# Optimization experiments

Hardware: AMD Instinct MI355X
Metric: run time of the kernel (lower is better)

## Reference

```python
import jax, jax.numpy as jnp
import numpy as np

N_NODES = 50000
N_EDGES = 800000
IN_DIM = 128
HID = 64
OUT = 64
HEADS = 4
NEG_SLOPE = 0.2  # DGL GATConv default leaky_relu negative slope


def gat_conv(x, src, dst, W, attn_l, attn_r, bias, n_heads, d_out, n_nodes):
    """DGL-style GATConv: x [N, F_in] -> [N, H, D]."""
    feat = (x @ W).reshape(n_nodes, n_heads, d_out)            # [N,H,D]
    el = jnp.sum(feat * attn_l, axis=-1)                        # [N,H]
    er = jnp.sum(feat * attn_r, axis=-1)                        # [N,H]
    e = jax.nn.leaky_relu(el[src] + er[dst], NEG_SLOPE)         # [E,H]
    # edge softmax over incoming edges of each dst node
    emax = jax.ops.segment_max(e, dst, num_segments=n_nodes)    # [N,H]
    emax = jnp.where(jnp.isfinite(emax), emax, 0.0)
    emax = jax.lax.stop_gradient(emax)
    a = jnp.exp(e - emax[dst])                                  # [E,H]
    denom = jax.ops.segment_sum(a, dst, num_segments=n_nodes)   # [N,H]
    alpha = a / jnp.maximum(denom[dst], 1e-9)                   # [E,H]
    msg = feat[src] * alpha[:, :, None]                         # [E,H,D]
    out = jax.ops.segment_sum(msg, dst, num_segments=n_nodes)   # [N,H,D]
    return out + bias.reshape(1, n_heads, d_out)


def setup_inputs() -> dict:
    key = jax.random.key(0)
    ks = jax.random.split(key, 12)
    features = jax.random.normal(ks[0], (N_NODES, IN_DIM), jnp.float32)
    src = jax.random.randint(ks[1], (N_EDGES,), 0, N_NODES)
    dst = jax.random.randint(ks[2], (N_EDGES,), 0, N_NODES)
    s1 = 1.0 / np.sqrt(IN_DIM)
    s2 = 1.0 / np.sqrt(HID * HEADS)
    return {
        "features": features,
        "src": src,
        "dst": dst,
        "W1": jax.random.normal(ks[3], (IN_DIM, HEADS * HID), jnp.float32) * s1,
        "al1": jax.random.normal(ks[4], (HEADS, HID), jnp.float32) * s1,
        "ar1": jax.random.normal(ks[5], (HEADS, HID), jnp.float32) * s1,
        "b1": jnp.zeros((HEADS * HID,), jnp.float32),
        "W2": jax.random.normal(ks[6], (HEADS * HID, HEADS * OUT), jnp.float32) * s2,
        "al2": jax.random.normal(ks[7], (HEADS, OUT), jnp.float32) * s2,
        "ar2": jax.random.normal(ks[8], (HEADS, OUT), jnp.float32) * s2,
        "b2": jnp.zeros((HEADS * OUT,), jnp.float32),
    }


def reference(features, src, dst, W1, al1, ar1, b1, W2, al2, ar2, b2):
    h = gat_conv(features, src, dst, W1, al1, ar1, b1, HEADS, HID, N_NODES)
    h = jax.nn.elu(h)                        # layer1 activation=F.elu
    h = h.reshape(N_NODES, HEADS * HID)      # .flatten(1)
    # dropout(0.2) is identity in eval mode
    h = gat_conv(h, src, dst, W2, al2, ar2, b2, HEADS, OUT, N_NODES)
    return h.mean(axis=1)                    # mean over heads -> [N, OUT]
```

## Files before the change

kernel.cpp:

```cpp
#include <hip/hip_runtime.h>
#include <hip/hip_bf16.h>
#include <math.h>

#define N_NODES 50000
#define N_EDGES 800000
#define IN_DIM 128
#define NEG_SLOPE 0.2f

typedef __attribute__((ext_vector_type(8))) short s16x8;
typedef __attribute__((ext_vector_type(4))) float f32x4;

__device__ inline unsigned short f2bf(float v) {
    unsigned u = __float_as_uint(v);
    unsigned r = (u + 0x7fffu + ((u >> 16) & 1u)) >> 16;
    return (unsigned short)r;
}
__device__ inline float bf2f(unsigned short b) {
    return __uint_as_float(((unsigned)b) << 16);
}
__device__ inline float lrelu(float v) {
    return v >= 0.f ? v : NEG_SLOPE * v;
}


__global__ void zero_int(int* __restrict__ p, int n) {
    int i = blockIdx.x * blockDim.x + threadIdx.x;
    if (i < n) p[i] = 0;
}

__global__ void hist_kernel(const int* __restrict__ dst, int* __restrict__ cnt) {
    int e = blockIdx.x * blockDim.x + threadIdx.x;
    if (e < N_EDGES) atomicAdd(&cnt[dst[e]], 1);
}

__global__ __launch_bounds__(1024) void scan_kernel(const int* __restrict__ cnt,
                                                    int* __restrict__ off, int n) {
    __shared__ int wsum[16];
    __shared__ int carry_s;
    int tid = threadIdx.x, wid = tid >> 6, lane = tid & 63;
    if (tid == 0) carry_s = 0;
    __syncthreads();
    for (int base = 0; base < n; base += 1024) {
        int i = base + tid;
        int v = (i < n) ? cnt[i] : 0;
        int x = v;
#pragma unroll
        for (int s = 1; s < 64; s <<= 1) {
            int t = __shfl_up(x, s, 64);
            if (lane >= s) x += t;
        }
        if (lane == 63) wsum[wid] = x;
        __syncthreads();
        if (wid == 0 && lane < 16) {
            int w = wsum[lane];
#pragma unroll
            for (int s = 1; s < 16; s <<= 1) {
                int t = __shfl_up(w, s, 64);
                if (lane >= s) w += t;
            }
            wsum[lane] = w;
        }
        __syncthreads();
        int woff = (wid > 0) ? wsum[wid - 1] : 0;
        int incl = carry_s + woff + x;
        if (i < n) off[i] = incl - v;
        __syncthreads();
        if (tid == 1023) carry_s = incl;
        __syncthreads();
    }
    if (threadIdx.x == 0) off[n] = carry_s;
}

__global__ void copy_int(const int* __restrict__ a, int* __restrict__ b, int n) {
    int i = blockIdx.x * blockDim.x + threadIdx.x;
    if (i < n) b[i] = a[i];
}

__global__ void scatter_kernel(const int* __restrict__ src, const int* __restrict__ dst,
                               int* __restrict__ cur, int* __restrict__ csr_src) {
    int e = blockIdx.x * blockDim.x + threadIdx.x;
    if (e < N_EDGES) {
        int d = dst[e];
        int pos = atomicAdd(&cur[d], 1);
        csr_src[pos] = src[e];
    }
}

template <int K>
__global__ void split_wt(const float* __restrict__ W, unsigned short* __restrict__ Bth,
                         unsigned short* __restrict__ Btl) {
    int k = blockIdx.x;
    int c = threadIdx.x;
    float v = W[(size_t)k * 256 + c];
    unsigned short h = f2bf(v);
    Bth[(size_t)c * K + k] = h;
    Btl[(size_t)c * K + k] = f2bf(v - bf2f(h));
}


template <int K, bool AF32>
__global__ __launch_bounds__(256) void mfma_gemm(const void* __restrict__ A_,
                                                 const unsigned short* __restrict__ Alo,
                                                 const unsigned short* __restrict__ Bth,
                                                 const unsigned short* __restrict__ Btl,
                                                 const float* __restrict__ attl,
                                                 const float* __restrict__ attr,
                                                 unsigned short* __restrict__ Chi,
                                                 float* __restrict__ el,
                                                 float* __restrict__ er,
                                                 int M) {
    int h = threadIdx.x >> 6;
    int lane = threadIdx.x & 63;
    int r = lane & 15;
    int g = lane >> 4;
    int kg = g * 8;
    int row0 = blockIdx.x * 32;

    f32x4 acc[2][4] = {};

    int rowA0 = row0 + r;      if (rowA0 >= M) rowA0 = M - 1;
    int rowA1 = row0 + 16 + r; if (rowA1 >= M) rowA1 = M - 1;

    const float* Af = (const float*)A_;
    const unsigned short* Ah = (const unsigned short*)A_;
    const unsigned short* pbh = Bth + (size_t)(h * 64 + r) * K + kg;
    const unsigned short* pbl = Btl + (size_t)(h * 64 + r) * K + kg;

#pragma unroll
    for (int kb = 0; kb < K; kb += 32) {
        s16x8 ah0, ah1, al0, al1;
        if (AF32) {
            const float* p0 = Af + (size_t)rowA0 * K + kb + kg;
            const float* p1 = Af + (size_t)rowA1 * K + kb + kg;
            float4 f00 = *reinterpret_cast<const float4*>(p0);
            float4 f01 = *reinterpret_cast<const float4*>(p0 + 4);
            float4 f10 = *reinterpret_cast<const float4*>(p1);
            float4 f11 = *reinterpret_cast<const float4*>(p1 + 4);
            float v0[8] = {f00.x, f00.y, f00.z, f00.w, f01.x, f01.y, f01.z, f01.w};
            float v1[8] = {f10.x, f10.y, f10.z, f10.w, f11.x, f11.y, f11.z, f11.w};
#pragma unroll
            for (int i = 0; i < 8; i++) {
                unsigned short hh0 = f2bf(v0[i]);
                unsigned short hh1 = f2bf(v1[i]);
                ah0[i] = (short)hh0; al0[i] = (short)f2bf(v0[i] - bf2f(hh0));
                ah1[i] = (short)hh1; al1[i] = (short)f2bf(v1[i] - bf2f(hh1));
            }
        } else {
            ah0 = *reinterpret_cast<const s16x8*>(Ah  + (size_t)rowA0 * K + kb + kg);
            ah1 = *reinterpret_cast<const s16x8*>(Ah  + (size_t)rowA1 * K + kb + kg);
            al0 = *reinterpret_cast<const s16x8*>(Alo + (size_t)rowA0 * K + kb + kg);
            al1 = *reinterpret_cast<const s16x8*>(Alo + (size_t)rowA1 * K + kb + kg);
        }
        s16x8 bh[4], bl[4];
#pragma unroll
        for (int ni = 0; ni < 4; ni++) {
            bh[ni] = *reinterpret_cast<const s16x8*>(pbh + (size_t)(ni * 16) * K + kb);
            bl[ni] = *reinterpret_cast<const s16x8*>(pbl + (size_t)(ni * 16) * K + kb);
        }
#pragma unroll
        for (int ni = 0; ni < 4; ni++) {
            acc[0][ni] = __builtin_amdgcn_mfma_f32_16x16x32_bf16(ah0, bh[ni], acc[0][ni], 0, 0, 0);
            acc[1][ni] = __builtin_amdgcn_mfma_f32_16x16x32_bf16(ah1, bh[ni], acc[1][ni], 0, 0, 0);
            acc[0][ni] = __builtin_amdgcn_mfma_f32_16x16x32_bf16(ah0, bl[ni], acc[0][ni], 0, 0, 0);
            acc[1][ni] = __builtin_amdgcn_mfma_f32_16x16x32_bf16(ah1, bl[ni], acc[1][ni], 0, 0, 0);
            acc[0][ni] = __builtin_amdgcn_mfma_f32_16x16x32_bf16(al0, bh[ni], acc[0][ni], 0, 0, 0);
            acc[1][ni] = __builtin_amdgcn_mfma_f32_16x16x32_bf16(al1, bh[ni], acc[1][ni], 0, 0, 0);
        }
    }

    float alv[4], arv[4];
#pragma unroll
    for (int ni = 0; ni < 4; ni++) {
        alv[ni] = attl[h * 64 + ni * 16 + r];
        arv[ni] = attr[h * 64 + ni * 16 + r];
    }
#pragma unroll
    for (int mi = 0; mi < 2; mi++) {
#pragma unroll
        for (int reg = 0; reg < 4; reg++) {
            int row = row0 + mi * 16 + g * 4 + reg;
            bool ok = row < M;
            float pel = 0.f, per_ = 0.f;
#pragma unroll
            for (int ni = 0; ni < 4; ni++) {
                float v = acc[mi][ni][reg];
                pel += v * alv[ni];
                per_ += v * arv[ni];
                if (ok) Chi[(size_t)row * 256 + h * 64 + ni * 16 + r] = f2bf(v);
            }
#pragma unroll
            for (int s = 1; s < 16; s <<= 1) {
                pel  += __shfl_xor(pel, s, 64);
                per_ += __shfl_xor(per_, s, 64);
            }
            if (r == 0 && ok) {
                el[row * 4 + h] = pel;
                er[row * 4 + h] = per_;
            }
        }
    }
}


template <int LAYER>
__global__ __launch_bounds__(256) void agg_kernel(const unsigned short* __restrict__ feat16,
                                                  const float* __restrict__ el,
                                                  const float* __restrict__ er,
                                                  const int* __restrict__ row_off,
                                                  const int* __restrict__ csr_src,
                                                  const float* __restrict__ bias,
                                                  unsigned short* __restrict__ out_hi,
                                                  unsigned short* __restrict__ out_lo,
                                                  float* __restrict__ outf) {
    int n = blockIdx.x * 4 + (threadIdx.x >> 6);
    int lane = threadIdx.x & 63;
    int h = lane >> 4;
    int js = row_off[n], je = row_off[n + 1];
    float er_nh = er[n * 4 + h];
    float m = -INFINITY, ssum = 0.f;
    float4 acc = make_float4(0.f, 0.f, 0.f, 0.f);
    int j = js;
    for (; j + 3 < je; j += 4) {
        int s0 = csr_src[j], s1 = csr_src[j + 1], s2 = csr_src[j + 2], s3 = csr_src[j + 3];
        ushort4 u0 = *reinterpret_cast<const ushort4*>(&feat16[(size_t)s0 * 256 + lane * 4]);
        ushort4 u1 = *reinterpret_cast<const ushort4*>(&feat16[(size_t)s1 * 256 + lane * 4]);
        ushort4 u2 = *reinterpret_cast<const ushort4*>(&feat16[(size_t)s2 * 256 + lane * 4]);
        ushort4 u3 = *reinterpret_cast<const ushort4*>(&feat16[(size_t)s3 * 256 + lane * 4]);
        float v0 = lrelu(el[s0 * 4 + h] + er_nh);
        float v1 = lrelu(el[s1 * 4 + h] + er_nh);
        float v2 = lrelu(el[s2 * 4 + h] + er_nh);
        float v3 = lrelu(el[s3 * 4 + h] + er_nh);
        float mx = fmaxf(fmaxf(v0, v1), fmaxf(v2, v3));
        float mn = fmaxf(m, mx);
        float sc = __expf(m - mn);
        float p0 = __expf(v0 - mn);
        float p1 = __expf(v1 - mn);
        float p2 = __expf(v2 - mn);
        float p3 = __expf(v3 - mn);
        ssum = ssum * sc + ((p0 + p1) + (p2 + p3));
        acc.x = acc.x * sc + (p0 * bf2f(u0.x) + p1 * bf2f(u1.x)) + (p2 * bf2f(u2.x) + p3 * bf2f(u3.x));
        acc.y = acc.y * sc + (p0 * bf2f(u0.y) + p1 * bf2f(u1.y)) + (p2 * bf2f(u2.y) + p3 * bf2f(u3.y));
        acc.z = acc.z * sc + (p0 * bf2f(u0.z) + p1 * bf2f(u1.z)) + (p2 * bf2f(u2.z) + p3 * bf2f(u3.z));
        acc.w = acc.w * sc + (p0 * bf2f(u0.w) + p1 * bf2f(u1.w)) + (p2 * bf2f(u2.w) + p3 * bf2f(u3.w));
        m = mn;
    }
    for (; j < je; j++) {
        int s = csr_src[j];
        ushort4 u = *reinterpret_cast<const ushort4*>(&feat16[(size_t)s * 256 + lane * 4]);
        float val = lrelu(el[s * 4 + h] + er_nh);
        float mn = fmaxf(m, val);
        float sc = __expf(m - mn);
        float p = __expf(val - mn);
        ssum = ssum * sc + p;
        acc.x = acc.x * sc + p * bf2f(u.x);
        acc.y = acc.y * sc + p * bf2f(u.y);
        acc.z = acc.z * sc + p * bf2f(u.z);
        acc.w = acc.w * sc + p * bf2f(u.w);
        m = mn;
    }
    float inv = 1.f / fmaxf(ssum, 1e-9f);
    float4 res;
    res.x = acc.x * inv + bias[lane * 4 + 0];
    res.y = acc.y * inv + bias[lane * 4 + 1];
    res.z = acc.z * inv + bias[lane * 4 + 2];
    res.w = acc.w * inv + bias[lane * 4 + 3];
    if (LAYER == 1) {
        res.x = res.x > 0.f ? res.x : __expf(res.x) - 1.f;
        res.y = res.y > 0.f ? res.y : __expf(res.y) - 1.f;
        res.z = res.z > 0.f ? res.z : __expf(res.z) - 1.f;
        res.w = res.w > 0.f ? res.w : __expf(res.w) - 1.f;
        ushort4 hz, lz;
        hz.x = f2bf(res.x); lz.x = f2bf(res.x - bf2f(hz.x));
        hz.y = f2bf(res.y); lz.y = f2bf(res.y - bf2f(hz.y));
        hz.z = f2bf(res.z); lz.z = f2bf(res.z - bf2f(hz.z));
        hz.w = f2bf(res.w); lz.w = f2bf(res.w - bf2f(hz.w));
        *reinterpret_cast<ushort4*>(&out_hi[(size_t)n * 256 + lane * 4]) = hz;
        *reinterpret_cast<ushort4*>(&out_lo[(size_t)n * 256 + lane * 4]) = lz;
    } else {
#pragma unroll
        for (int mask = 16; mask <= 32; mask <<= 1) {
            res.x += __shfl_xor(res.x, mask, 64);
            res.y += __shfl_xor(res.y, mask, 64);
            res.z += __shfl_xor(res.z, mask, 64);
            res.w += __shfl_xor(res.w, mask, 64);
        }
        if (lane < 16) {
            float4 o = make_float4(res.x * 0.25f, res.y * 0.25f, res.z * 0.25f, res.w * 0.25f);
            *reinterpret_cast<float4*>(&outf[(size_t)n * 64 + lane * 4]) = o;
        }
    }
}


extern "C" void kernel_launch(void* const* d_in, const int* in_sizes, int n_in,
                              void* d_out, int out_size, void* d_ws, size_t ws_size,
                              hipStream_t stream) {
    const float* features = (const float*)d_in[0];
    const int*   src      = (const int*)d_in[1];
    const int*   dst      = (const int*)d_in[2];
    const float* W1       = (const float*)d_in[3];
    const float* al1      = (const float*)d_in[4];
    const float* ar1      = (const float*)d_in[5];
    const float* b1       = (const float*)d_in[6];
    const float* W2       = (const float*)d_in[7];
    const float* al2      = (const float*)d_in[8];
    const float* ar2      = (const float*)d_in[9];
    const float* b2       = (const float*)d_in[10];
    float* out = (float*)d_out;

    char* ws = (char*)d_ws;
    unsigned short* feat16  = (unsigned short*)(ws);
    unsigned short* h1_hi   = (unsigned short*)(ws + 25600000);
    unsigned short* h1_lo   = (unsigned short*)(ws + 51200000);
    unsigned short* Bt1_hi  = (unsigned short*)(ws + 76800000);
    unsigned short* Bt1_lo  = (unsigned short*)(ws + 76865536);
    unsigned short* Bt2_hi  = (unsigned short*)(ws + 76931072);
    unsigned short* Bt2_lo  = (unsigned short*)(ws + 77062144);
    float*          el      = (float*)(ws + 77193216);
    float*          er      = (float*)(ws + 77993216);
    int*            row_off = (int*)  (ws + 78793216);
    int*            cur     = (int*)  (ws + 78993280);
    int*            csr     = (int*)  (ws + 79193280);

    zero_int<<<(N_NODES + 255) / 256, 256, 0, stream>>>(cur, N_NODES);
    hist_kernel<<<(N_EDGES + 255) / 256, 256, 0, stream>>>(dst, cur);
    scan_kernel<<<1, 1024, 0, stream>>>(cur, row_off, N_NODES);
    copy_int<<<(N_NODES + 255) / 256, 256, 0, stream>>>(row_off, cur, N_NODES);
    scatter_kernel<<<(N_EDGES + 255) / 256, 256, 0, stream>>>(src, dst, cur, csr);

    split_wt<IN_DIM><<<IN_DIM, 256, 0, stream>>>(W1, Bt1_hi, Bt1_lo);
    split_wt<256><<<256, 256, 0, stream>>>(W2, Bt2_hi, Bt2_lo);

    int gemm_blocks = (N_NODES + 31) / 32;

    mfma_gemm<IN_DIM, true><<<gemm_blocks, 256, 0, stream>>>(
        features, nullptr, Bt1_hi, Bt1_lo, al1, ar1, feat16, el, er, N_NODES);
    agg_kernel<1><<<12500, 256, 0, stream>>>(feat16, el, er, row_off, csr, b1, h1_hi, h1_lo, nullptr);

    mfma_gemm<256, false><<<gemm_blocks, 256, 0, stream>>>(
        h1_hi, h1_lo, Bt2_hi, Bt2_lo, al2, ar2, feat16, el, er, N_NODES);
    agg_kernel<2><<<12500, 256, 0, stream>>>(feat16, el, er, row_off, csr, b2, nullptr, nullptr, out);
}
```

Measured before the change: 398.5 us.

## Stage GEMM tiles in double-buffered LDS, pre-split features, unroll aggregation by eight

```diff
diff --git a/kernel.cpp b/kernel.cpp
--- a/kernel.cpp
+++ b/kernel.cpp
@@ -86,6 +86,22 @@
     }
 }
 
+
+__global__ void split_feat(const float* __restrict__ in, unsigned short* __restrict__ hi,
+                           unsigned short* __restrict__ lo, int n4) {
+    int i = blockIdx.x * blockDim.x + threadIdx.x;
+    if (i < n4) {
+        float4 v = *reinterpret_cast<const float4*>(&in[i * 4]);
+        ushort4 h, l;
+        h.x = f2bf(v.x); l.x = f2bf(v.x - bf2f(h.x));
+        h.y = f2bf(v.y); l.y = f2bf(v.y - bf2f(h.y));
+        h.z = f2bf(v.z); l.z = f2bf(v.z - bf2f(h.z));
+        h.w = f2bf(v.w); l.w = f2bf(v.w - bf2f(h.w));
+        *reinterpret_cast<ushort4*>(&hi[i * 4]) = h;
+        *reinterpret_cast<ushort4*>(&lo[i * 4]) = l;
+    }
+}
+
 template <int K>
 __global__ void split_wt(const float* __restrict__ W, unsigned short* __restrict__ Bth,
                          unsigned short* __restrict__ Btl) {
@@ -98,84 +114,98 @@
 }
 
 
-template <int K, bool AF32>
-__global__ __launch_bounds__(256) void mfma_gemm(const void* __restrict__ A_,
-                                                 const unsigned short* __restrict__ Alo,
-                                                 const unsigned short* __restrict__ Bth,
-                                                 const unsigned short* __restrict__ Btl,
-                                                 const float* __restrict__ attl,
-                                                 const float* __restrict__ attr,
-                                                 unsigned short* __restrict__ Chi,
-                                                 float* __restrict__ el,
-                                                 float* __restrict__ er,
-                                                 int M) {
-    int h = threadIdx.x >> 6;
-    int lane = threadIdx.x & 63;
-    int r = lane & 15;
+#define GLDS(gsrc, loff)                                                        \
+    __builtin_amdgcn_global_load_lds(                                           \
+        (const __attribute__((address_space(1))) unsigned int*)(gsrc),          \
+        (__attribute__((address_space(3))) unsigned int*)(lds + (loff)),        \
+        16, 0, 0)
+
+template <int K>
+__global__ __launch_bounds__(256, 2) void mfma_gemm(const unsigned short* __restrict__ Ahi,
+                                                    const unsigned short* __restrict__ Alo,
+                                                    const unsigned short* __restrict__ Bth,
+                                                    const unsigned short* __restrict__ Btl,
+                                                    const float* __restrict__ attl,
+                                                    const float* __restrict__ attr,
+                                                    unsigned short* __restrict__ Chi,
+                                                    float* __restrict__ el,
+                                                    float* __restrict__ er,
+                                                    int M) {
+    __shared__ __align__(16) char lds[81920];
+    int tid = threadIdx.x;
+    int h = tid >> 6;
+    int lane = tid & 63;
+    int rr = lane & 15;
     int g = lane >> 4;
-    int kg = g * 8;
-    int row0 = blockIdx.x * 32;
-
-    f32x4 acc[2][4] = {};
-
-    int rowA0 = row0 + r;      if (rowA0 >= M) rowA0 = M - 1;
-    int rowA1 = row0 + 16 + r; if (rowA1 >= M) rowA1 = M - 1;
-
-    const float* Af = (const float*)A_;
-    const unsigned short* Ah = (const unsigned short*)A_;
-    const unsigned short* pbh = Bth + (size_t)(h * 64 + r) * K + kg;
-    const unsigned short* pbl = Btl + (size_t)(h * 64 + r) * K + kg;
-
-#pragma unroll
+    int row0 = blockIdx.x * 64;
+
+    int arow = row0 + (tid & 63);
+    if (arow >= M) arow = M - 1;
+    int akc = tid >> 6;
+    const unsigned short* asrc_h = Ahi + (size_t)arow * K + akc * 8;
+    const unsigned short* asrc_l = Alo + (size_t)arow * K + akc * 8;
+    const unsigned short* bsrc_h = Bth + (size_t)tid * K;
+    const unsigned short* bsrc_l = Btl + (size_t)tid * K;
+
+    f32x4 acc[4][4] = {};
+
+    {
+        GLDS(asrc_h, tid * 16);
+        GLDS(asrc_l, 4096 + tid * 16);
+#pragma unroll
+        for (int j = 0; j < 4; j++) {
+            GLDS(bsrc_h + j * 8, 8192 + j * 4096 + tid * 16);
+            GLDS(bsrc_l + j * 8, 24576 + j * 4096 + tid * 16);
+        }
+    }
+
+    int cur = 0;
     for (int kb = 0; kb < K; kb += 32) {
-        s16x8 ah0, ah1, al0, al1;
-        if (AF32) {
-            const float* p0 = Af + (size_t)rowA0 * K + kb + kg;
-            const float* p1 = Af + (size_t)rowA1 * K + kb + kg;
-            float4 f00 = *reinterpret_cast<const float4*>(p0);
-            float4 f01 = *reinterpret_cast<const float4*>(p0 + 4);
-            float4 f10 = *reinterpret_cast<const float4*>(p1);
-            float4 f11 = *reinterpret_cast<const float4*>(p1 + 4);
-            float v0[8] = {f00.x, f00.y, f00.z, f00.w, f01.x, f01.y, f01.z, f01.w};
-            float v1[8] = {f10.x, f10.y, f10.z, f10.w, f11.x, f11.y, f11.z, f11.w};
-#pragma unroll
-            for (int i = 0; i < 8; i++) {
-                unsigned short hh0 = f2bf(v0[i]);
-                unsigned short hh1 = f2bf(v1[i]);
-                ah0[i] = (short)hh0; al0[i] = (short)f2bf(v0[i] - bf2f(hh0));
-                ah1[i] = (short)hh1; al1[i] = (short)f2bf(v1[i] - bf2f(hh1));
-            }
-        } else {
-            ah0 = *reinterpret_cast<const s16x8*>(Ah  + (size_t)rowA0 * K + kb + kg);
-            ah1 = *reinterpret_cast<const s16x8*>(Ah  + (size_t)rowA1 * K + kb + kg);
-            al0 = *reinterpret_cast<const s16x8*>(Alo + (size_t)rowA0 * K + kb + kg);
-            al1 = *reinterpret_cast<const s16x8*>(Alo + (size_t)rowA1 * K + kb + kg);
-        }
-        s16x8 bh[4], bl[4];
+        __syncthreads();
+        if (kb + 32 < K) {
+            int nb = (cur ^ 1) * 40960;
+            GLDS(asrc_h + kb + 32, nb + tid * 16);
+            GLDS(asrc_l + kb + 32, nb + 4096 + tid * 16);
+#pragma unroll
+            for (int j = 0; j < 4; j++) {
+                GLDS(bsrc_h + kb + 32 + j * 8, nb + 8192 + j * 4096 + tid * 16);
+                GLDS(bsrc_l + kb + 32 + j * 8, nb + 24576 + j * 4096 + tid * 16);
+            }
+        }
+        const char* lb = lds + cur * 40960;
+        s16x8 ah[4], al[4], bh[4], bl[4];
+#pragma unroll
+        for (int mi = 0; mi < 4; mi++) {
+            int off = g * 1024 + (mi * 16 + rr) * 16;
+            ah[mi] = *reinterpret_cast<const s16x8*>(lb + off);
+            al[mi] = *reinterpret_cast<const s16x8*>(lb + 4096 + off);
+        }
 #pragma unroll
         for (int ni = 0; ni < 4; ni++) {
-            bh[ni] = *reinterpret_cast<const s16x8*>(pbh + (size_t)(ni * 16) * K + kb);
-            bl[ni] = *reinterpret_cast<const s16x8*>(pbl + (size_t)(ni * 16) * K + kb);
-        }
-#pragma unroll
-        for (int ni = 0; ni < 4; ni++) {
-            acc[0][ni] = __builtin_amdgcn_mfma_f32_16x16x32_bf16(ah0, bh[ni], acc[0][ni], 0, 0, 0);
-            acc[1][ni] = __builtin_amdgcn_mfma_f32_16x16x32_bf16(ah1, bh[ni], acc[1][ni], 0, 0, 0);
-            acc[0][ni] = __builtin_amdgcn_mfma_f32_16x16x32_bf16(ah0, bl[ni], acc[0][ni], 0, 0, 0);
-            acc[1][ni] = __builtin_amdgcn_mfma_f32_16x16x32_bf16(ah1, bl[ni], acc[1][ni], 0, 0, 0);
-            acc[0][ni] = __builtin_amdgcn_mfma_f32_16x16x32_bf16(al0, bh[ni], acc[0][ni], 0, 0, 0);
-            acc[1][ni] = __builtin_amdgcn_mfma_f32_16x16x32_bf16(al1, bh[ni], acc[1][ni], 0, 0, 0);
-        }
+            int off = g * 4096 + (h * 64 + ni * 16 + rr) * 16;
+            bh[ni] = *reinterpret_cast<const s16x8*>(lb + 8192 + off);
+            bl[ni] = *reinterpret_cast<const s16x8*>(lb + 24576 + off);
+        }
+#pragma unroll
+        for (int mi = 0; mi < 4; mi++) {
+#pragma unroll
+            for (int ni = 0; ni < 4; ni++) {
+                acc[mi][ni] = __builtin_amdgcn_mfma_f32_16x16x32_bf16(ah[mi], bh[ni], acc[mi][ni], 0, 0, 0);
+                acc[mi][ni] = __builtin_amdgcn_mfma_f32_16x16x32_bf16(ah[mi], bl[ni], acc[mi][ni], 0, 0, 0);
+                acc[mi][ni] = __builtin_amdgcn_mfma_f32_16x16x32_bf16(al[mi], bh[ni], acc[mi][ni], 0, 0, 0);
+            }
+        }
+        cur ^= 1;
     }
 
     float alv[4], arv[4];
 #pragma unroll
     for (int ni = 0; ni < 4; ni++) {
-        alv[ni] = attl[h * 64 + ni * 16 + r];
-        arv[ni] = attr[h * 64 + ni * 16 + r];
-    }
-#pragma unroll
-    for (int mi = 0; mi < 2; mi++) {
+        alv[ni] = attl[h * 64 + ni * 16 + rr];
+        arv[ni] = attr[h * 64 + ni * 16 + rr];
+    }
+#pragma unroll
+    for (int mi = 0; mi < 4; mi++) {
 #pragma unroll
         for (int reg = 0; reg < 4; reg++) {
             int row = row0 + mi * 16 + g * 4 + reg;
@@ -186,14 +216,14 @@
                 float v = acc[mi][ni][reg];
                 pel += v * alv[ni];
                 per_ += v * arv[ni];
-                if (ok) Chi[(size_t)row * 256 + h * 64 + ni * 16 + r] = f2bf(v);
+                if (ok) Chi[(size_t)row * 256 + h * 64 + ni * 16 + rr] = f2bf(v);
             }
 #pragma unroll
             for (int s = 1; s < 16; s <<= 1) {
                 pel  += __shfl_xor(pel, s, 64);
                 per_ += __shfl_xor(per_, s, 64);
             }
-            if (r == 0 && ok) {
+            if (rr == 0 && ok) {
                 el[row * 4 + h] = pel;
                 er[row * 4 + h] = per_;
             }
@@ -220,6 +250,38 @@
     float m = -INFINITY, ssum = 0.f;
     float4 acc = make_float4(0.f, 0.f, 0.f, 0.f);
     int j = js;
+    for (; j + 7 < je; j += 8) {
+        int ss[8]; ushort4 uu[8]; float vv[8];
+#pragma unroll
+        for (int q = 0; q < 8; q++) ss[q] = csr_src[j + q];
+#pragma unroll
+        for (int q = 0; q < 8; q++)
+            uu[q] = *reinterpret_cast<const ushort4*>(&feat16[(size_t)ss[q] * 256 + lane * 4]);
+#pragma unroll
+        for (int q = 0; q < 8; q++) vv[q] = lrelu(el[ss[q] * 4 + h] + er_nh);
+        float mx = fmaxf(fmaxf(fmaxf(vv[0], vv[1]), fmaxf(vv[2], vv[3])),
+                         fmaxf(fmaxf(vv[4], vv[5]), fmaxf(vv[6], vv[7])));
+        float mn = fmaxf(m, mx);
+        float sc = __expf(m - mn);
+        float p[8];
+#pragma unroll
+        for (int q = 0; q < 8; q++) p[q] = __expf(vv[q] - mn);
+        float psum = ((p[0] + p[1]) + (p[2] + p[3])) + ((p[4] + p[5]) + (p[6] + p[7]));
+        ssum = ssum * sc + psum;
+        float ax = 0.f, ay = 0.f, az = 0.f, aw = 0.f;
+#pragma unroll
+        for (int q = 0; q < 8; q++) {
+            ax += p[q] * bf2f(uu[q].x);
+            ay += p[q] * bf2f(uu[q].y);
+            az += p[q] * bf2f(uu[q].z);
+            aw += p[q] * bf2f(uu[q].w);
+        }
+        acc.x = acc.x * sc + ax;
+        acc.y = acc.y * sc + ay;
+        acc.z = acc.z * sc + az;
+        acc.w = acc.w * sc + aw;
+        m = mn;
+    }
     for (; j + 3 < je; j += 4) {
         int s0 = csr_src[j], s1 = csr_src[j + 1], s2 = csr_src[j + 2], s3 = csr_src[j + 3];
         ushort4 u0 = *reinterpret_cast<const ushort4*>(&feat16[(size_t)s0 * 256 + lane * 4]);
@@ -312,15 +374,17 @@
     unsigned short* feat16  = (unsigned short*)(ws);
     unsigned short* h1_hi   = (unsigned short*)(ws + 25600000);
     unsigned short* h1_lo   = (unsigned short*)(ws + 51200000);
-    unsigned short* Bt1_hi  = (unsigned short*)(ws + 76800000);
-    unsigned short* Bt1_lo  = (unsigned short*)(ws + 76865536);
-    unsigned short* Bt2_hi  = (unsigned short*)(ws + 76931072);
-    unsigned short* Bt2_lo  = (unsigned short*)(ws + 77062144);
-    float*          el      = (float*)(ws + 77193216);
-    float*          er      = (float*)(ws + 77993216);
-    int*            row_off = (int*)  (ws + 78793216);
-    int*            cur     = (int*)  (ws + 78993280);
-    int*            csr     = (int*)  (ws + 79193280);
+    unsigned short* fA_hi   = (unsigned short*)(ws + 76800000);
+    unsigned short* fA_lo   = (unsigned short*)(ws + 89600000);
+    unsigned short* Bt1_hi  = (unsigned short*)(ws + 102400000);
+    unsigned short* Bt1_lo  = (unsigned short*)(ws + 102465536);
+    unsigned short* Bt2_hi  = (unsigned short*)(ws + 102531072);
+    unsigned short* Bt2_lo  = (unsigned short*)(ws + 102662144);
+    float*          el      = (float*)(ws + 102793216);
+    float*          er      = (float*)(ws + 103593216);
+    int*            row_off = (int*)  (ws + 104393216);
+    int*            cur     = (int*)  (ws + 104593280);
+    int*            csr     = (int*)  (ws + 104793280);
 
     zero_int<<<(N_NODES + 255) / 256, 256, 0, stream>>>(cur, N_NODES);
     hist_kernel<<<(N_EDGES + 255) / 256, 256, 0, stream>>>(dst, cur);
@@ -328,16 +392,18 @@
     copy_int<<<(N_NODES + 255) / 256, 256, 0, stream>>>(row_off, cur, N_NODES);
     scatter_kernel<<<(N_EDGES + 255) / 256, 256, 0, stream>>>(src, dst, cur, csr);
 
+    split_feat<<<(N_NODES * IN_DIM / 4 + 255) / 256, 256, 0, stream>>>(
+        features, fA_hi, fA_lo, N_NODES * IN_DIM / 4);
     split_wt<IN_DIM><<<IN_DIM, 256, 0, stream>>>(W1, Bt1_hi, Bt1_lo);
     split_wt<256><<<256, 256, 0, stream>>>(W2, Bt2_hi, Bt2_lo);
 
-    int gemm_blocks = (N_NODES + 31) / 32;
-
-    mfma_gemm<IN_DIM, true><<<gemm_blocks, 256, 0, stream>>>(
-        features, nullptr, Bt1_hi, Bt1_lo, al1, ar1, feat16, el, er, N_NODES);
+    int gemm_blocks = (N_NODES + 63) / 64;
+
+    mfma_gemm<IN_DIM><<<gemm_blocks, 256, 0, stream>>>(
+        fA_hi, fA_lo, Bt1_hi, Bt1_lo, al1, ar1, feat16, el, er, N_NODES);
     agg_kernel<1><<<12500, 256, 0, stream>>>(feat16, el, er, row_off, csr, b1, h1_hi, h1_lo, nullptr);
 
-    mfma_gemm<256, false><<<gemm_blocks, 256, 0, stream>>>(
+    mfma_gemm<256><<<gemm_blocks, 256, 0, stream>>>(
         h1_hi, h1_lo, Bt2_hi, Bt2_lo, al2, ar2, feat16, el, er, N_NODES);
     agg_kernel<2><<<12500, 256, 0, stream>>>(feat16, el, er, row_off, csr, b2, nullptr, nullptr, out);
 }
```

New measurement: 401.0 us. No clear change (+0.6%).

## Fold attention vectors into GEMM weights, vectorize feature stores, unroll aggregation by eight

Applied to the files above, without the earlier changes.

```diff
diff --git a/kernel.cpp b/kernel.cpp
--- a/kernel.cpp
+++ b/kernel.cpp
@@ -86,15 +86,45 @@
     }
 }
 
+
 template <int K>
 __global__ void split_wt(const float* __restrict__ W, unsigned short* __restrict__ Bth,
                          unsigned short* __restrict__ Btl) {
     int k = blockIdx.x;
     int c = threadIdx.x;
+    int h = c >> 6, w = c & 63;
+    int row = h * 64 + (w & 3) * 16 + (w >> 2);
     float v = W[(size_t)k * 256 + c];
-    unsigned short h = f2bf(v);
-    Bth[(size_t)c * K + k] = h;
-    Btl[(size_t)c * K + k] = f2bf(v - bf2f(h));
+    unsigned short hh = f2bf(v);
+    Bth[(size_t)row * K + k] = hh;
+    Btl[(size_t)row * K + k] = f2bf(v - bf2f(hh));
+}
+
+template <int K>
+__global__ void wlr_kernel(const float* __restrict__ W, const float* __restrict__ al,
+                           const float* __restrict__ ar,
+                           unsigned short* __restrict__ Eh, unsigned short* __restrict__ El) {
+    int k = blockIdx.x * blockDim.x + threadIdx.x;
+    if (k >= K) return;
+#pragma unroll
+    for (int h = 0; h < 4; h++) {
+        float sl = 0.f, sr = 0.f;
+        for (int c = 0; c < 64; c++) {
+            float w = W[(size_t)k * 256 + h * 64 + c];
+            sl += w * al[h * 64 + c];
+            sr += w * ar[h * 64 + c];
+        }
+        unsigned short hh = f2bf(sl);
+        Eh[(size_t)(h * 16 + 0) * K + k] = hh;
+        El[(size_t)(h * 16 + 0) * K + k] = f2bf(sl - bf2f(hh));
+        hh = f2bf(sr);
+        Eh[(size_t)(h * 16 + 1) * K + k] = hh;
+        El[(size_t)(h * 16 + 1) * K + k] = f2bf(sr - bf2f(hh));
+        for (int j = 2; j < 16; j++) {
+            Eh[(size_t)(h * 16 + j) * K + k] = 0;
+            El[(size_t)(h * 16 + j) * K + k] = 0;
+        }
+    }
 }
 
 
@@ -103,28 +133,31 @@
                                                  const unsigned short* __restrict__ Alo,
                                                  const unsigned short* __restrict__ Bth,
                                                  const unsigned short* __restrict__ Btl,
-                                                 const float* __restrict__ attl,
-                                                 const float* __restrict__ attr,
+                                                 const unsigned short* __restrict__ Eh,
+                                                 const unsigned short* __restrict__ El_,
                                                  unsigned short* __restrict__ Chi,
                                                  float* __restrict__ el,
                                                  float* __restrict__ er,
                                                  int M) {
     int h = threadIdx.x >> 6;
     int lane = threadIdx.x & 63;
-    int r = lane & 15;
+    int rr = lane & 15;
     int g = lane >> 4;
     int kg = g * 8;
     int row0 = blockIdx.x * 32;
 
     f32x4 acc[2][4] = {};
-
-    int rowA0 = row0 + r;      if (rowA0 >= M) rowA0 = M - 1;
-    int rowA1 = row0 + 16 + r; if (rowA1 >= M) rowA1 = M - 1;
+    f32x4 acce[2] = {};
+
+    int rowA0 = row0 + rr;      if (rowA0 >= M) rowA0 = M - 1;
+    int rowA1 = row0 + 16 + rr; if (rowA1 >= M) rowA1 = M - 1;
 
     const float* Af = (const float*)A_;
     const unsigned short* Ah = (const unsigned short*)A_;
-    const unsigned short* pbh = Bth + (size_t)(h * 64 + r) * K + kg;
-    const unsigned short* pbl = Btl + (size_t)(h * 64 + r) * K + kg;
+    const unsigned short* pbh = Bth + (size_t)(h * 64 + rr) * K + kg;
+    const unsigned short* pbl = Btl + (size_t)(h * 64 + rr) * K + kg;
+    const unsigned short* peh = Eh  + (size_t)(h * 16 + rr) * K + kg;
+    const unsigned short* pel = El_ + (size_t)(h * 16 + rr) * K + kg;
 
 #pragma unroll
     for (int kb = 0; kb < K; kb += 32) {
@@ -157,6 +190,8 @@
             bh[ni] = *reinterpret_cast<const s16x8*>(pbh + (size_t)(ni * 16) * K + kb);
             bl[ni] = *reinterpret_cast<const s16x8*>(pbl + (size_t)(ni * 16) * K + kb);
         }
+        s16x8 beh = *reinterpret_cast<const s16x8*>(peh + kb);
+        s16x8 bel = *reinterpret_cast<const s16x8*>(pel + kb);
 #pragma unroll
         for (int ni = 0; ni < 4; ni++) {
             acc[0][ni] = __builtin_amdgcn_mfma_f32_16x16x32_bf16(ah0, bh[ni], acc[0][ni], 0, 0, 0);
@@ -166,36 +201,28 @@
             acc[0][ni] = __builtin_amdgcn_mfma_f32_16x16x32_bf16(al0, bh[ni], acc[0][ni], 0, 0, 0);
             acc[1][ni] = __builtin_amdgcn_mfma_f32_16x16x32_bf16(al1, bh[ni], acc[1][ni], 0, 0, 0);
         }
-    }
-
-    float alv[4], arv[4];
-#pragma unroll
-    for (int ni = 0; ni < 4; ni++) {
-        alv[ni] = attl[h * 64 + ni * 16 + r];
-        arv[ni] = attr[h * 64 + ni * 16 + r];
-    }
+        acce[0] = __builtin_amdgcn_mfma_f32_16x16x32_bf16(ah0, beh, acce[0], 0, 0, 0);
+        acce[1] = __builtin_amdgcn_mfma_f32_16x16x32_bf16(ah1, beh, acce[1], 0, 0, 0);
+        acce[0] = __builtin_amdgcn_mfma_f32_16x16x32_bf16(ah0, bel, acce[0], 0, 0, 0);
+        acce[1] = __builtin_amdgcn_mfma_f32_16x16x32_bf16(ah1, bel, acce[1], 0, 0, 0);
+        acce[0] = __builtin_amdgcn_mfma_f32_16x16x32_bf16(al0, beh, acce[0], 0, 0, 0);
+        acce[1] = __builtin_amdgcn_mfma_f32_16x16x32_bf16(al1, beh, acce[1], 0, 0, 0);
+    }
+
 #pragma unroll
     for (int mi = 0; mi < 2; mi++) {
 #pragma unroll
         for (int reg = 0; reg < 4; reg++) {
             int row = row0 + mi * 16 + g * 4 + reg;
-            bool ok = row < M;
-            float pel = 0.f, per_ = 0.f;
-#pragma unroll
-            for (int ni = 0; ni < 4; ni++) {
-                float v = acc[mi][ni][reg];
-                pel += v * alv[ni];
-                per_ += v * arv[ni];
-                if (ok) Chi[(size_t)row * 256 + h * 64 + ni * 16 + r] = f2bf(v);
-            }
-#pragma unroll
-            for (int s = 1; s < 16; s <<= 1) {
-                pel  += __shfl_xor(pel, s, 64);
-                per_ += __shfl_xor(per_, s, 64);
-            }
-            if (r == 0 && ok) {
-                el[row * 4 + h] = pel;
-                er[row * 4 + h] = per_;
+            if (row < M) {
+                ushort4 u;
+                u.x = f2bf(acc[mi][0][reg]);
+                u.y = f2bf(acc[mi][1][reg]);
+                u.z = f2bf(acc[mi][2][reg]);
+                u.w = f2bf(acc[mi][3][reg]);
+                *reinterpret_cast<ushort4*>(&Chi[(size_t)row * 256 + h * 64 + rr * 4]) = u;
+                if (rr == 0) el[row * 4 + h] = acce[mi][reg];
+                if (rr == 1) er[row * 4 + h] = acce[mi][reg];
             }
         }
     }
@@ -220,6 +247,38 @@
     float m = -INFINITY, ssum = 0.f;
     float4 acc = make_float4(0.f, 0.f, 0.f, 0.f);
     int j = js;
+    for (; j + 7 < je; j += 8) {
+        int ss[8]; ushort4 uu[8]; float vv[8];
+#pragma unroll
+        for (int q = 0; q < 8; q++) ss[q] = csr_src[j + q];
+#pragma unroll
+        for (int q = 0; q < 8; q++)
+            uu[q] = *reinterpret_cast<const ushort4*>(&feat16[(size_t)ss[q] * 256 + lane * 4]);
+#pragma unroll
+        for (int q = 0; q < 8; q++) vv[q] = lrelu(el[ss[q] * 4 + h] + er_nh);
+        float mx = fmaxf(fmaxf(fmaxf(vv[0], vv[1]), fmaxf(vv[2], vv[3])),
+                         fmaxf(fmaxf(vv[4], vv[5]), fmaxf(vv[6], vv[7])));
+        float mn = fmaxf(m, mx);
+        float sc = __expf(m - mn);
+        float p[8];
+#pragma unroll
+        for (int q = 0; q < 8; q++) p[q] = __expf(vv[q] - mn);
+        float psum = ((p[0] + p[1]) + (p[2] + p[3])) + ((p[4] + p[5]) + (p[6] + p[7]));
+        ssum = ssum * sc + psum;
+        float ax = 0.f, ay = 0.f, az = 0.f, aw = 0.f;
+#pragma unroll
+        for (int q = 0; q < 8; q++) {
+            ax += p[q] * bf2f(uu[q].x);
+            ay += p[q] * bf2f(uu[q].y);
+            az += p[q] * bf2f(uu[q].z);
+            aw += p[q] * bf2f(uu[q].w);
+        }
+        acc.x = acc.x * sc + ax;
+        acc.y = acc.y * sc + ay;
+        acc.z = acc.z * sc + az;
+        acc.w = acc.w * sc + aw;
+        m = mn;
+    }
     for (; j + 3 < je; j += 4) {
         int s0 = csr_src[j], s1 = csr_src[j + 1], s2 = csr_src[j + 2], s3 = csr_src[j + 3];
         ushort4 u0 = *reinterpret_cast<const ushort4*>(&feat16[(size_t)s0 * 256 + lane * 4]);
@@ -316,11 +375,15 @@
     unsigned short* Bt1_lo  = (unsigned short*)(ws + 76865536);
     unsigned short* Bt2_hi  = (unsigned short*)(ws + 76931072);
     unsigned short* Bt2_lo  = (unsigned short*)(ws + 77062144);
-    float*          el      = (float*)(ws + 77193216);
-    float*          er      = (float*)(ws + 77993216);
-    int*            row_off = (int*)  (ws + 78793216);
-    int*            cur     = (int*)  (ws + 78993280);
-    int*            csr     = (int*)  (ws + 79193280);
+    unsigned short* E1_hi   = (unsigned short*)(ws + 77193216);
+    unsigned short* E1_lo   = (unsigned short*)(ws + 77209600);
+    unsigned short* E2_hi   = (unsigned short*)(ws + 77225984);
+    unsigned short* E2_lo   = (unsigned short*)(ws + 77258752);
+    float*          el      = (float*)(ws + 77291520);
+    float*          er      = (float*)(ws + 78091520);
+    int*            row_off = (int*)  (ws + 78891520);
+    int*            cur     = (int*)  (ws + 79091584);
+    int*            csr     = (int*)  (ws + 79291584);
 
     zero_int<<<(N_NODES + 255) / 256, 256, 0, stream>>>(cur, N_NODES);
     hist_kernel<<<(N_EDGES + 255) / 256, 256, 0, stream>>>(dst, cur);
@@ -330,14 +393,16 @@
 
     split_wt<IN_DIM><<<IN_DIM, 256, 0, stream>>>(W1, Bt1_hi, Bt1_lo);
     split_wt<256><<<256, 256, 0, stream>>>(W2, Bt2_hi, Bt2_lo);
+    wlr_kernel<IN_DIM><<<1, 256, 0, stream>>>(W1, al1, ar1, E1_hi, E1_lo);
+    wlr_kernel<256><<<1, 256, 0, stream>>>(W2, al2, ar2, E2_hi, E2_lo);
 
     int gemm_blocks = (N_NODES + 31) / 32;
 
     mfma_gemm<IN_DIM, true><<<gemm_blocks, 256, 0, stream>>>(
-        features, nullptr, Bt1_hi, Bt1_lo, al1, ar1, feat16, el, er, N_NODES);
+        features, nullptr, Bt1_hi, Bt1_lo, E1_hi, E1_lo, feat16, el, er, N_NODES);
     agg_kernel<1><<<12500, 256, 0, stream>>>(feat16, el, er, row_off, csr, b1, h1_hi, h1_lo, nullptr);
 
     mfma_gemm<256, false><<<gemm_blocks, 256, 0, stream>>>(
-        h1_hi, h1_lo, Bt2_hi, Bt2_lo, al2, ar2, feat16, el, er, N_NODES);
+        h1_hi, h1_lo, Bt2_hi, Bt2_lo, E2_hi, E2_lo, feat16, el, er, N_NODES);
     agg_kernel<2><<<12500, 256, 0, stream>>>(feat16, el, er, row_off, csr, b2, nullptr, nullptr, out);
 }
```

Result: slower. 441.7 us (+10.9%).
